# Kernel tuning notes

Hardware: AMD Instinct MI355X
Metric: run time of the kernel (lower is better)

The kernel has to match this reference:

```python
import jax, jax.numpy as jnp
import numpy as np
import math

HEAD_DIM = 128
THETA = 10000.0
MASK_VAL = -10000.0


def _rope(x, cos, sin):
    # x: (B, S, D); cos/sin: (S, D//2). Pairs (even, odd) rotated as complex.
    xr = x.reshape(*x.shape[:-1], -1, 2)
    xe, xo = xr[..., 0], xr[..., 1]
    oe = xe * cos - xo * sin
    oo = xe * sin + xo * cos
    return jnp.stack([oe, oo], axis=-1).reshape(x.shape)


def setup_inputs() -> dict:
    key = jax.random.key(0)
    B, S, D = 8, 4096, HEAD_DIM
    qkv = jax.random.normal(key, (B, S, 3 * D), dtype=jnp.float32)
    return {"qkv": qkv}


def reference(qkv):
    B, S, threeD = qkv.shape
    D = threeD // 3
    qkv = qkv.reshape(B, S, 3, D)
    q, k, v = qkv[:, :, 0], qkv[:, :, 1], qkv[:, :, 2]

    # precompute_freqs_cis: outer(t, 1/theta^(2i/d)) -> cos/sin (S, D//2)
    inv_freq = 1.0 / (THETA ** (jnp.arange(0, D, 2, dtype=jnp.float32) / D))
    freqs = jnp.arange(S, dtype=jnp.float32)[:, None] * inv_freq[None, :]
    cos, sin = jnp.cos(freqs), jnp.sin(freqs)
    q = _rope(q, cos, sin)
    k = _rope(k, cos, sin)

    scale = 1.0 / math.sqrt(D)
    scores = jnp.einsum('btd,bsd->bts', q, k) * scale  # (B, S, S)
    causal_mask = jnp.triu(jnp.full((S, S), MASK_VAL, dtype=scores.dtype), 1)
    attn = jax.nn.softmax(scores + causal_mask, axis=-1)
    out = jnp.einsum('bts,bsd->btd', attn, v)  # (B, S, D)
    return out
```

## Files before the change

kernel.cpp:

```cpp
#include <hip/hip_runtime.h>
#include <math.h>

typedef _Float16 half8 __attribute__((ext_vector_type(8)));
typedef float floatx4 __attribute__((ext_vector_type(4)));
typedef float floatx2 __attribute__((ext_vector_type(2)));

#define B_ 8
#define S_ 4096
#define SCALE_L2E 0.12751743008389106f
#define MASK_L2E  -14426.950408889634f
#define L2_10K_OVER_128 0.10381025296522975f

#define PLD 72
#define KW  136
#define VW  24
#define OSTLD 136
#define SLOTS_PER_B 576

__device__ __forceinline__ int chunk_prefix(int qt32) {
    int g = qt32 >> 4;
    return qt32 + 8 * g * (g - 1) + (qt32 - (g << 4)) * g;
}

__global__ __launch_bounds__(256) void prep_kernel(const float* __restrict__ qkv,
                                                   _Float16* __restrict__ Qh,
                                                   _Float16* __restrict__ Kp,
                                                   _Float16* __restrict__ Vp) {
    __shared__ __align__(16) _Float16 Kl[16][KW];
    __shared__ __align__(16) _Float16 Vt[128][VW];
    const int tid = threadIdx.x;
    const int b   = blockIdx.y;
    const int s0  = blockIdx.x * 16;

#pragma unroll
    for (int it = 0; it < 4; ++it) {
        int idx = tid + it * 256;
        int i = idx & 63, sr = idx >> 6, s = s0 + sr;
        const float* base = qkv + ((size_t)(b * S_ + s)) * 384 + 2 * i;
        floatx2 q2 = *(const floatx2*)base;
        floatx2 k2 = *(const floatx2*)(base + 128);
        float inv = exp2f(-(float)(2 * i) * L2_10K_OVER_128);
        float ang = (float)s * inv;
        float sn, cs;
        __sincosf(ang, &sn, &cs);
        size_t oq = ((size_t)(b * S_ + s)) * 128 + 2 * i;
        Qh[oq]     = (_Float16)((q2[0] * cs - q2[1] * sn) * SCALE_L2E);
        Qh[oq + 1] = (_Float16)((q2[0] * sn + q2[1] * cs) * SCALE_L2E);
        Kl[sr][2 * i]     = (_Float16)(k2[0] * cs - k2[1] * sn);
        Kl[sr][2 * i + 1] = (_Float16)(k2[0] * sn + k2[1] * cs);
    }
#pragma unroll
    for (int it = 0; it < 2; ++it) {
        int idx = tid + it * 256;
        int c = idx & 31, sr = idx >> 5;
        floatx4 v = *(const floatx4*)(qkv + ((size_t)(b * S_ + s0 + sr)) * 384 + 256 + c * 4);
#pragma unroll
        for (int j = 0; j < 4; ++j) Vt[c * 4 + j][sr] = (_Float16)v[j];
    }
    __syncthreads();

    {
        int c = tid >> 6, lane = tid & 63;
        int quad = lane >> 4, n = lane & 15;
        half8 val = *(const half8*)&Kl[n][c * 32 + quad * 8];
        int s16 = s0 >> 4;
        *(half8*)(Kp + (((size_t)(b * 256 + s16) * 4 + c) * 64 + lane) * 8) = val;
    }
    {
        int kt = s0 >> 6, c2 = (s0 >> 5) & 1, qp = (s0 >> 4) & 1;
        int nt = tid >> 5, lq = (tid >> 4) & 1, n = tid & 15;
        int quad = qp * 2 + lq;
        int lane = quad * 16 + n;
        half8 val = *(const half8*)&Vt[nt * 16 + n][lq * 8];
        *(half8*)(Vp + ((((size_t)(b * 64 + kt) * 2 + c2) * 8 + nt) * 64 + lane) * 8) = val;
    }
}

__global__ __launch_bounds__(64) void attn_part_kernel(const _Float16* __restrict__ Qh,
                                                       const _Float16* __restrict__ Kp,
                                                       const _Float16* __restrict__ Vp,
                                                       _Float16* __restrict__ Ppart,
                                                       float* __restrict__ Lpart) {
    __shared__ __align__(16) _Float16 SH[4 * 16 * PLD];

    const int lane  = threadIdx.x;
    const int quad  = lane >> 4;
    const int l16   = lane & 15;
    const int b     = blockIdx.x & 7;
    const int chunk = blockIdx.x >> 3;
    const int qt32  = 127 - blockIdx.y;
    const int qr0   = qt32 * 32;
    const int kt_max = (qr0 + 31) >> 6;
    const int c0    = chunk * 8;
    if (c0 > kt_max) return;
    const int kend  = min(kt_max, c0 + 7);
    const int slot  = b * SLOTS_PER_B + chunk_prefix(qt32) + chunk;

    half8 aq[2][4];
#pragma unroll
    for (int tile = 0; tile < 2; ++tile) {
        const _Float16* Qb = Qh + ((size_t)(b * S_) + qr0 + tile * 16 + l16) * 128;
#pragma unroll
        for (int c = 0; c < 4; ++c) aq[tile][c] = *(const half8*)(Qb + c * 32 + quad * 8);
    }

    floatx4 o[2][8];
#pragma unroll
    for (int tile = 0; tile < 2; ++tile)
#pragma unroll
        for (int i = 0; i < 8; ++i) o[tile][i] = (floatx4){0.f, 0.f, 0.f, 0.f};
    float rsum[2][4] = {{0.f, 0.f, 0.f, 0.f}, {0.f, 0.f, 0.f, 0.f}};

    const _Float16* Kb = Kp + (size_t)b * 524288;
    const _Float16* Vb = Vp + (size_t)b * 524288;

    for (int kt = c0; kt <= kend; ++kt) {
        floatx4 s4[2][4];
#pragma unroll
        for (int t = 0; t < 4; ++t) {
            const _Float16* kp = Kb + (((size_t)(kt * 16 + t * 4)) * 64 + lane) * 8;
            half8 bk[4];
#pragma unroll
            for (int c = 0; c < 4; ++c) bk[c] = *(const half8*)(kp + c * 512);
            floatx4 a0 = (floatx4){0.f, 0.f, 0.f, 0.f};
            floatx4 a1 = (floatx4){0.f, 0.f, 0.f, 0.f};
#pragma unroll
            for (int c = 0; c < 4; ++c) {
                a0 = __builtin_amdgcn_mfma_f32_16x16x32_f16(aq[0][c], bk[c], a0, 0, 0, 0);
                a1 = __builtin_amdgcn_mfma_f32_16x16x32_f16(aq[1][c], bk[c], a1, 0, 0, 0);
            }
            s4[0][t] = a0; s4[1][t] = a1;
        }

        if (kt == kt_max) {
#pragma unroll
            for (int tile = 0; tile < 2; ++tile)
#pragma unroll
                for (int t = 0; t < 4; ++t)
#pragma unroll
                    for (int r = 0; r < 4; ++r) {
                        int kcol = kt * 64 + t * 16 + l16;
                        int qr   = qr0 + tile * 16 + quad * 4 + r;
                        if (kcol > qr) s4[tile][t][r] += MASK_L2E;
                    }
        }

        const int buf = kt & 1;
#pragma unroll
        for (int tile = 0; tile < 2; ++tile)
#pragma unroll
            for (int t = 0; t < 4; ++t)
#pragma unroll
                for (int r = 0; r < 4; ++r) {
                    float p = __builtin_amdgcn_exp2f(s4[tile][t][r]);
                    rsum[tile][r] += p;
                    SH[(tile * 2 + buf) * (16 * PLD) + (quad * 4 + r) * PLD + t * 16 + l16] = (_Float16)p;
                }

#pragma unroll
        for (int c2 = 0; c2 < 2; ++c2) {
            half8 vf[8];
#pragma unroll
            for (int nt = 0; nt < 8; ++nt)
                vf[nt] = *(const half8*)(Vb + (((size_t)(kt * 2 + c2) * 8 + nt) * 64 + lane) * 8);
#pragma unroll
            for (int tile = 0; tile < 2; ++tile) {
                half8 ap = *(const half8*)&SH[(tile * 2 + buf) * (16 * PLD) + l16 * PLD + c2 * 32 + quad * 8];
#pragma unroll
                for (int nt = 0; nt < 8; ++nt)
                    o[tile][nt] = __builtin_amdgcn_mfma_f32_16x16x32_f16(ap, vf[nt], o[tile][nt], 0, 0, 0);
            }
        }
    }

#pragma unroll
    for (int off = 1; off <= 8; off <<= 1)
#pragma unroll
        for (int tile = 0; tile < 2; ++tile)
#pragma unroll
            for (int r = 0; r < 4; ++r)
                rsum[tile][r] += __shfl_xor(rsum[tile][r], off, 64);
    if (l16 == 0) {
#pragma unroll
        for (int tile = 0; tile < 2; ++tile)
#pragma unroll
            for (int r = 0; r < 4; ++r)
                Lpart[(size_t)slot * 32 + tile * 16 + quad * 4 + r] = rsum[tile][r];
    }

    _Float16* Ost = SH;
#pragma unroll
    for (int tile = 0; tile < 2; ++tile)
#pragma unroll
        for (int nt = 0; nt < 8; ++nt)
#pragma unroll
            for (int r = 0; r < 4; ++r)
                Ost[(tile * 16 + quad * 4 + r) * OSTLD + nt * 16 + l16] = (_Float16)o[tile][nt][r];
    _Float16* pp = Ppart + (size_t)slot * 4096;
#pragma unroll
    for (int i = 0; i < 8; ++i) {
        int idx = lane + i * 64;
        half8 v = *(const half8*)&Ost[(idx >> 4) * OSTLD + (idx & 15) * 8];
        *(half8*)(pp + (size_t)idx * 8) = v;
    }
}

__global__ __launch_bounds__(256) void reduce_kernel(const _Float16* __restrict__ Ppart,
                                                     const float* __restrict__ Lpart,
                                                     float* __restrict__ out) {
    const int bid  = blockIdx.x;
    const int b    = bid >> 7;
    const int qt32 = bid & 127;
    const int qr0  = qt32 * 32;
    const int nch  = (((qr0 + 31) >> 6) >> 3) + 1;
    const int slot0 = b * SLOTS_PER_B + chunk_prefix(qt32);
    const _Float16* pp = Ppart + (size_t)slot0 * 4096;
    const float* lp = Lpart + (size_t)slot0 * 32;
    const int tid = threadIdx.x;

#pragma unroll
    for (int j = 0; j < 2; ++j) {
        int idx = tid + j * 256;
        int row = idx >> 4;
        float acc[8] = {0.f, 0.f, 0.f, 0.f, 0.f, 0.f, 0.f, 0.f};
        float l = 0.f;
        for (int c = 0; c < nch; ++c) {
            half8 v = *(const half8*)(pp + (size_t)c * 4096 + (size_t)idx * 8);
#pragma unroll
            for (int k = 0; k < 8; ++k) acc[k] += (float)v[k];
            l += lp[c * 32 + row];
        }
        float inv = 1.0f / l;
        float* ob = out + ((size_t)(b * S_) + qr0) * 128 + (size_t)idx * 8;
        floatx4 o0 = (floatx4){acc[0] * inv, acc[1] * inv, acc[2] * inv, acc[3] * inv};
        floatx4 o1 = (floatx4){acc[4] * inv, acc[5] * inv, acc[6] * inv, acc[7] * inv};
        *(floatx4*)ob = o0;
        *(floatx4*)(ob + 4) = o1;
    }
}

__global__ __launch_bounds__(64) void attn_atomic_kernel(const _Float16* __restrict__ Qh,
                                                         const _Float16* __restrict__ Kp,
                                                         const _Float16* __restrict__ Vp,
                                                         float* __restrict__ out,
                                                         float* __restrict__ Lg) {
    __shared__ __align__(16) _Float16 Pl[2][16 * PLD];
    const int lane = threadIdx.x, quad = lane >> 4, l16 = lane & 15;
    const int b = blockIdx.x & 7, chunk = blockIdx.x >> 3;
    const int qt = 255 - blockIdx.y, qr0 = qt * 16;
    const int kt_max = qt >> 2, c0 = chunk * 8;
    if (c0 > kt_max) return;
    const int kend = min(kt_max, c0 + 7);
    const _Float16* Qb = Qh + ((size_t)(b * S_) + qr0 + l16) * 128;
    half8 aq[4];
#pragma unroll
    for (int c = 0; c < 4; ++c) aq[c] = *(const half8*)(Qb + c * 32 + quad * 8);
    floatx4 o[8];
#pragma unroll
    for (int i = 0; i < 8; ++i) o[i] = (floatx4){0.f, 0.f, 0.f, 0.f};
    float rsum[4] = {0.f, 0.f, 0.f, 0.f};
    const _Float16* Kb = Kp + (size_t)b * 524288;
    const _Float16* Vb = Vp + (size_t)b * 524288;
    for (int kt = c0; kt <= kend; ++kt) {
        half8 vf[2][8];
#pragma unroll
        for (int c2 = 0; c2 < 2; ++c2)
#pragma unroll
            for (int nt = 0; nt < 8; ++nt)
                vf[c2][nt] = *(const half8*)(Vb + (((size_t)(kt * 2 + c2) * 8 + nt) * 64 + lane) * 8);
        floatx4 s4[4];
#pragma unroll
        for (int t = 0; t < 4; ++t) {
            const _Float16* kp = Kb + ((size_t)((kt * 4 + t) * 4) * 64 + lane) * 8;
            floatx4 acc = (floatx4){0.f, 0.f, 0.f, 0.f};
#pragma unroll
            for (int c = 0; c < 4; ++c) {
                half8 bk = *(const half8*)(kp + c * 512);
                acc = __builtin_amdgcn_mfma_f32_16x16x32_f16(aq[c], bk, acc, 0, 0, 0);
            }
            s4[t] = acc;
        }
        if (kt == kt_max) {
#pragma unroll
            for (int t = 0; t < 4; ++t)
#pragma unroll
                for (int r = 0; r < 4; ++r) {
                    int kcol = kt * 64 + t * 16 + l16;
                    int qr = qr0 + quad * 4 + r;
                    if (kcol > qr) s4[t][r] += MASK_L2E;
                }
        }
        const int buf = kt & 1;
#pragma unroll
        for (int t = 0; t < 4; ++t)
#pragma unroll
            for (int r = 0; r < 4; ++r) {
                float p = __builtin_amdgcn_exp2f(s4[t][r]);
                rsum[r] += p;
                Pl[buf][(quad * 4 + r) * PLD + t * 16 + l16] = (_Float16)p;
            }
#pragma unroll
        for (int c2 = 0; c2 < 2; ++c2) {
            half8 ap = *(const half8*)&Pl[buf][l16 * PLD + c2 * 32 + quad * 8];
#pragma unroll
            for (int nt = 0; nt < 8; ++nt)
                o[nt] = __builtin_amdgcn_mfma_f32_16x16x32_f16(ap, vf[c2][nt], o[nt], 0, 0, 0);
        }
    }
#pragma unroll
    for (int off = 1; off <= 8; off <<= 1)
#pragma unroll
        for (int r = 0; r < 4; ++r)
            rsum[r] += __shfl_xor(rsum[r], off, 64);
    if (l16 == 0) {
#pragma unroll
        for (int r = 0; r < 4; ++r)
            atomicAdd(&Lg[(size_t)(b * S_) + qr0 + quad * 4 + r], rsum[r]);
    }
    float* ob = out + ((size_t)(b * S_) + qr0) * 128;
#pragma unroll
    for (int nt = 0; nt < 8; ++nt)
#pragma unroll
        for (int r = 0; r < 4; ++r)
            atomicAdd(&ob[(quad * 4 + r) * 128 + nt * 16 + l16], o[nt][r]);
}

__global__ __launch_bounds__(256) void norm_kernel(float* __restrict__ out,
                                                   const float* __restrict__ Lg) {
    int i = blockIdx.x * 256 + threadIdx.x;
    int row = i >> 5;
    floatx4 v = *(floatx4*)(out + (size_t)i * 4);
    float inv = 1.0f / Lg[row];
    v[0] *= inv; v[1] *= inv; v[2] *= inv; v[3] *= inv;
    *(floatx4*)(out + (size_t)i * 4) = v;
}

extern "C" void kernel_launch(void* const* d_in, const int* in_sizes, int n_in,
                              void* d_out, int out_size, void* d_ws, size_t ws_size,
                              hipStream_t stream) {
    const float* qkv = (const float*)d_in[0];
    float* out = (float*)d_out;
    const size_t MB = 1024 * 1024;
    _Float16* Qh = (_Float16*)d_ws;
    _Float16* Kp = (_Float16*)((char*)d_ws + 8 * MB);
    _Float16* Vp = (_Float16*)((char*)d_ws + 16 * MB);

    const size_t lpart_bytes = (size_t)B_ * SLOTS_PER_B * 32 * sizeof(float);
    const size_t ppart_bytes = (size_t)B_ * SLOTS_PER_B * 4096 * sizeof(_Float16);
    const size_t need = 25 * MB + ppart_bytes;

    prep_kernel<<<dim3(256, B_), dim3(256), 0, stream>>>(qkv, Qh, Kp, Vp);

    if (ws_size >= need) {
        float*    Lpart = (float*)((char*)d_ws + 24 * MB);
        _Float16* Ppart = (_Float16*)((char*)d_ws + 25 * MB);
        (void)lpart_bytes;
        attn_part_kernel<<<dim3(64, 128), dim3(64), 0, stream>>>(Qh, Kp, Vp, Ppart, Lpart);
        reduce_kernel<<<dim3(1024), dim3(256), 0, stream>>>(Ppart, Lpart, out);
    } else {
        float* Lg = (float*)((char*)d_ws + 24 * MB);
        hipMemsetAsync(out, 0, (size_t)B_ * S_ * 128 * sizeof(float), stream);
        hipMemsetAsync(Lg, 0, (size_t)B_ * S_ * sizeof(float), stream);
        attn_atomic_kernel<<<dim3(64, 256), dim3(64), 0, stream>>>(Qh, Kp, Vp, out, Lg);
        norm_kernel<<<dim3(4096), dim3(256), 0, stream>>>(out, Lg);
    }
}
```

Measured before the change: 167.9 us.

## Pack four attention waves per block and widen prep to 32 rows

The attention partial kernel now runs four independent 64-lane waves per 256-thread block. Each wave gets its own shared-memory slice and takes its batch/chunk from blockIdx.x*4+wid, so there are fewer blocks to launch and the work lands on compute units more densely. The double-buffered P staging is dropped to a single buffer per wave, and the output staging is done one tile at a time to fit that smaller slice. The prep kernel now handles 32 rows per 512-thread block, which lets V be written out as full 32-row fragments. Waves in a block exit early on their own, so some blocks may sit partly idle, and the single P buffer removes any overlap between writing P and reading it.

```diff
diff --git a/kernel.cpp b/kernel.cpp
--- a/kernel.cpp
+++ b/kernel.cpp
@@ -13,7 +13,7 @@
 
 #define PLD 72
 #define KW  136
-#define VW  24
+#define VW  40
 #define OSTLD 136
 #define SLOTS_PER_B 576
 
@@ -22,19 +22,19 @@
     return qt32 + 8 * g * (g - 1) + (qt32 - (g << 4)) * g;
 }
 
-__global__ __launch_bounds__(256) void prep_kernel(const float* __restrict__ qkv,
+__global__ __launch_bounds__(512) void prep_kernel(const float* __restrict__ qkv,
                                                    _Float16* __restrict__ Qh,
                                                    _Float16* __restrict__ Kp,
                                                    _Float16* __restrict__ Vp) {
-    __shared__ __align__(16) _Float16 Kl[16][KW];
+    __shared__ __align__(16) _Float16 Kl[32][KW];
     __shared__ __align__(16) _Float16 Vt[128][VW];
     const int tid = threadIdx.x;
     const int b   = blockIdx.y;
-    const int s0  = blockIdx.x * 16;
+    const int s0  = blockIdx.x * 32;
 
 #pragma unroll
     for (int it = 0; it < 4; ++it) {
-        int idx = tid + it * 256;
+        int idx = tid + it * 512;
         int i = idx & 63, sr = idx >> 6, s = s0 + sr;
         const float* base = qkv + ((size_t)(b * S_ + s)) * 384 + 2 * i;
         floatx2 q2 = *(const floatx2*)base;
@@ -51,7 +51,7 @@
     }
 #pragma unroll
     for (int it = 0; it < 2; ++it) {
-        int idx = tid + it * 256;
+        int idx = tid + it * 512;
         int c = idx & 31, sr = idx >> 5;
         floatx4 v = *(const floatx4*)(qkv + ((size_t)(b * S_ + s0 + sr)) * 384 + 256 + c * 4);
 #pragma unroll
@@ -60,34 +60,36 @@
     __syncthreads();
 
     {
-        int c = tid >> 6, lane = tid & 63;
+        int t = tid >> 8, c = (tid >> 6) & 3, lane = tid & 63;
         int quad = lane >> 4, n = lane & 15;
-        half8 val = *(const half8*)&Kl[n][c * 32 + quad * 8];
-        int s16 = s0 >> 4;
+        half8 val = *(const half8*)&Kl[t * 16 + n][c * 32 + quad * 8];
+        int s16 = (s0 >> 4) + t;
         *(half8*)(Kp + (((size_t)(b * 256 + s16) * 4 + c) * 64 + lane) * 8) = val;
     }
     {
-        int kt = s0 >> 6, c2 = (s0 >> 5) & 1, qp = (s0 >> 4) & 1;
-        int nt = tid >> 5, lq = (tid >> 4) & 1, n = tid & 15;
-        int quad = qp * 2 + lq;
-        int lane = quad * 16 + n;
-        half8 val = *(const half8*)&Vt[nt * 16 + n][lq * 8];
+        int kt = s0 >> 6, c2 = (s0 >> 5) & 1;
+        int nt = tid >> 6, lane = tid & 63;
+        int quad = lane >> 4, n = lane & 15;
+        half8 val = *(const half8*)&Vt[nt * 16 + n][quad * 8];
         *(half8*)(Vp + ((((size_t)(b * 64 + kt) * 2 + c2) * 8 + nt) * 64 + lane) * 8) = val;
     }
 }
 
-__global__ __launch_bounds__(64) void attn_part_kernel(const _Float16* __restrict__ Qh,
-                                                       const _Float16* __restrict__ Kp,
-                                                       const _Float16* __restrict__ Vp,
-                                                       _Float16* __restrict__ Ppart,
-                                                       float* __restrict__ Lpart) {
-    __shared__ __align__(16) _Float16 SH[4 * 16 * PLD];
-
-    const int lane  = threadIdx.x;
+__global__ __launch_bounds__(256) void attn_part_kernel(const _Float16* __restrict__ Qh,
+                                                        const _Float16* __restrict__ Kp,
+                                                        const _Float16* __restrict__ Vp,
+                                                        _Float16* __restrict__ Ppart,
+                                                        float* __restrict__ Lpart) {
+    __shared__ __align__(16) _Float16 SH[4][2 * 16 * PLD];
+
+    const int tid   = threadIdx.x;
+    const int wid   = tid >> 6;
+    const int lane  = tid & 63;
     const int quad  = lane >> 4;
     const int l16   = lane & 15;
-    const int b     = blockIdx.x & 7;
-    const int chunk = blockIdx.x >> 3;
+    const int ux    = blockIdx.x * 4 + wid;
+    const int b     = ux >> 3;
+    const int chunk = ux & 7;
     const int qt32  = 127 - blockIdx.y;
     const int qr0   = qt32 * 32;
     const int kt_max = (qr0 + 31) >> 6;
@@ -95,6 +97,7 @@
     if (c0 > kt_max) return;
     const int kend  = min(kt_max, c0 + 7);
     const int slot  = b * SLOTS_PER_B + chunk_prefix(qt32) + chunk;
+    _Float16* sh = SH[wid];
 
     half8 aq[2][4];
 #pragma unroll
@@ -145,7 +148,6 @@
                     }
         }
 
-        const int buf = kt & 1;
 #pragma unroll
         for (int tile = 0; tile < 2; ++tile)
 #pragma unroll
@@ -154,7 +156,7 @@
                 for (int r = 0; r < 4; ++r) {
                     float p = __builtin_amdgcn_exp2f(s4[tile][t][r]);
                     rsum[tile][r] += p;
-                    SH[(tile * 2 + buf) * (16 * PLD) + (quad * 4 + r) * PLD + t * 16 + l16] = (_Float16)p;
+                    sh[tile * (16 * PLD) + (quad * 4 + r) * PLD + t * 16 + l16] = (_Float16)p;
                 }
 
 #pragma unroll
@@ -165,7 +167,7 @@
                 vf[nt] = *(const half8*)(Vb + (((size_t)(kt * 2 + c2) * 8 + nt) * 64 + lane) * 8);
 #pragma unroll
             for (int tile = 0; tile < 2; ++tile) {
-                half8 ap = *(const half8*)&SH[(tile * 2 + buf) * (16 * PLD) + l16 * PLD + c2 * 32 + quad * 8];
+                half8 ap = *(const half8*)&sh[tile * (16 * PLD) + l16 * PLD + c2 * 32 + quad * 8];
 #pragma unroll
                 for (int nt = 0; nt < 8; ++nt)
                     o[tile][nt] = __builtin_amdgcn_mfma_f32_16x16x32_f16(ap, vf[nt], o[tile][nt], 0, 0, 0);
@@ -188,20 +190,21 @@
                 Lpart[(size_t)slot * 32 + tile * 16 + quad * 4 + r] = rsum[tile][r];
     }
 
-    _Float16* Ost = SH;
-#pragma unroll
-    for (int tile = 0; tile < 2; ++tile)
+    _Float16* Ost = sh;
+    _Float16* pp = Ppart + (size_t)slot * 4096;
+#pragma unroll
+    for (int tile = 0; tile < 2; ++tile) {
 #pragma unroll
         for (int nt = 0; nt < 8; ++nt)
 #pragma unroll
             for (int r = 0; r < 4; ++r)
-                Ost[(tile * 16 + quad * 4 + r) * OSTLD + nt * 16 + l16] = (_Float16)o[tile][nt][r];
-    _Float16* pp = Ppart + (size_t)slot * 4096;
-#pragma unroll
-    for (int i = 0; i < 8; ++i) {
-        int idx = lane + i * 64;
-        half8 v = *(const half8*)&Ost[(idx >> 4) * OSTLD + (idx & 15) * 8];
-        *(half8*)(pp + (size_t)idx * 8) = v;
+                Ost[(quad * 4 + r) * OSTLD + nt * 16 + l16] = (_Float16)o[tile][nt][r];
+#pragma unroll
+        for (int i = 0; i < 4; ++i) {
+            int idx = lane + i * 64;
+            half8 v = *(const half8*)&Ost[(idx >> 4) * OSTLD + (idx & 15) * 8];
+            *(half8*)(pp + (size_t)(tile * 2048 + idx * 8)) = v;
+        }
     }
 }
 
@@ -345,17 +348,15 @@
     _Float16* Kp = (_Float16*)((char*)d_ws + 8 * MB);
     _Float16* Vp = (_Float16*)((char*)d_ws + 16 * MB);
 
-    const size_t lpart_bytes = (size_t)B_ * SLOTS_PER_B * 32 * sizeof(float);
     const size_t ppart_bytes = (size_t)B_ * SLOTS_PER_B * 4096 * sizeof(_Float16);
     const size_t need = 25 * MB + ppart_bytes;
 
-    prep_kernel<<<dim3(256, B_), dim3(256), 0, stream>>>(qkv, Qh, Kp, Vp);
+    prep_kernel<<<dim3(128, B_), dim3(512), 0, stream>>>(qkv, Qh, Kp, Vp);
 
     if (ws_size >= need) {
         float*    Lpart = (float*)((char*)d_ws + 24 * MB);
         _Float16* Ppart = (_Float16*)((char*)d_ws + 25 * MB);
-        (void)lpart_bytes;
-        attn_part_kernel<<<dim3(64, 128), dim3(64), 0, stream>>>(Qh, Kp, Vp, Ppart, Lpart);
+        attn_part_kernel<<<dim3(16, 128), dim3(256), 0, stream>>>(Qh, Kp, Vp, Ppart, Lpart);
         reduce_kernel<<<dim3(1024), dim3(256), 0, stream>>>(Ppart, Lpart, out);
     } else {
         float* Lg = (float*)((char*)d_ws + 24 * MB);
```

New measurement: 194.1 us. 1.16x slower.

## Group four query tiles per block and prefetch V before QK compute

Applied to the files above, without the earlier changes.

Each block now runs four waves, each handling one 32-row query tile from a group of four consecutive tiles that share a key range, so K/V tiles are reused across waves through cache. V fragments for a key tile are loaded before the QK MFMAs to hide load latency. Waves whose diagonal lies earlier still iterate to the block's last key tile with masking, which adds some wasted MFMA and exp work. Output staging through LDS is done per tile to fit four per-wave buffers.

```diff
diff --git a/kernel.cpp b/kernel.cpp
--- a/kernel.cpp
+++ b/kernel.cpp
@@ -76,25 +76,31 @@
     }
 }
 
-__global__ __launch_bounds__(64) void attn_part_kernel(const _Float16* __restrict__ Qh,
-                                                       const _Float16* __restrict__ Kp,
-                                                       const _Float16* __restrict__ Vp,
-                                                       _Float16* __restrict__ Ppart,
-                                                       float* __restrict__ Lpart) {
-    __shared__ __align__(16) _Float16 SH[4 * 16 * PLD];
-
-    const int lane  = threadIdx.x;
+__global__ __launch_bounds__(256) void attn_part_kernel(const _Float16* __restrict__ Qh,
+                                                        const _Float16* __restrict__ Kp,
+                                                        const _Float16* __restrict__ Vp,
+                                                        _Float16* __restrict__ Ppart,
+                                                        float* __restrict__ Lpart) {
+    __shared__ __align__(16) _Float16 SH[4][4 * 16 * PLD];
+
+    const int tid   = threadIdx.x;
+    const int wid   = tid >> 6;
+    const int lane  = tid & 63;
     const int quad  = lane >> 4;
     const int l16   = lane & 15;
     const int b     = blockIdx.x & 7;
     const int chunk = blockIdx.x >> 3;
-    const int qt32  = 127 - blockIdx.y;
+    const int Q     = 31 - blockIdx.y;
+    const int nch   = (Q >> 2) + 1;
+    if (chunk >= nch) return;
+    const int qt32  = Q * 4 + wid;
     const int qr0   = qt32 * 32;
-    const int kt_max = (qr0 + 31) >> 6;
+    const int my_ktmax  = qt32 >> 1;
+    const int blk_ktmax = 2 * Q + 1;
     const int c0    = chunk * 8;
-    if (c0 > kt_max) return;
-    const int kend  = min(kt_max, c0 + 7);
+    const int kend  = min(blk_ktmax, c0 + 7);
     const int slot  = b * SLOTS_PER_B + chunk_prefix(qt32) + chunk;
+    _Float16* sh = SH[wid];
 
     half8 aq[2][4];
 #pragma unroll
@@ -115,6 +121,13 @@
     const _Float16* Vb = Vp + (size_t)b * 524288;
 
     for (int kt = c0; kt <= kend; ++kt) {
+        half8 vf[2][8];
+#pragma unroll
+        for (int c2 = 0; c2 < 2; ++c2)
+#pragma unroll
+            for (int nt = 0; nt < 8; ++nt)
+                vf[c2][nt] = *(const half8*)(Vb + (((size_t)(kt * 2 + c2) * 8 + nt) * 64 + lane) * 8);
+
         floatx4 s4[2][4];
 #pragma unroll
         for (int t = 0; t < 4; ++t) {
@@ -132,7 +145,7 @@
             s4[0][t] = a0; s4[1][t] = a1;
         }
 
-        if (kt == kt_max) {
+        if (kt >= my_ktmax) {
 #pragma unroll
             for (int tile = 0; tile < 2; ++tile)
 #pragma unroll
@@ -154,21 +167,17 @@
                 for (int r = 0; r < 4; ++r) {
                     float p = __builtin_amdgcn_exp2f(s4[tile][t][r]);
                     rsum[tile][r] += p;
-                    SH[(tile * 2 + buf) * (16 * PLD) + (quad * 4 + r) * PLD + t * 16 + l16] = (_Float16)p;
+                    sh[(tile * 2 + buf) * (16 * PLD) + (quad * 4 + r) * PLD + t * 16 + l16] = (_Float16)p;
                 }
 
 #pragma unroll
         for (int c2 = 0; c2 < 2; ++c2) {
-            half8 vf[8];
-#pragma unroll
-            for (int nt = 0; nt < 8; ++nt)
-                vf[nt] = *(const half8*)(Vb + (((size_t)(kt * 2 + c2) * 8 + nt) * 64 + lane) * 8);
 #pragma unroll
             for (int tile = 0; tile < 2; ++tile) {
-                half8 ap = *(const half8*)&SH[(tile * 2 + buf) * (16 * PLD) + l16 * PLD + c2 * 32 + quad * 8];
+                half8 ap = *(const half8*)&sh[(tile * 2 + buf) * (16 * PLD) + l16 * PLD + c2 * 32 + quad * 8];
 #pragma unroll
                 for (int nt = 0; nt < 8; ++nt)
-                    o[tile][nt] = __builtin_amdgcn_mfma_f32_16x16x32_f16(ap, vf[nt], o[tile][nt], 0, 0, 0);
+                    o[tile][nt] = __builtin_amdgcn_mfma_f32_16x16x32_f16(ap, vf[c2][nt], o[tile][nt], 0, 0, 0);
             }
         }
     }
@@ -188,20 +197,21 @@
                 Lpart[(size_t)slot * 32 + tile * 16 + quad * 4 + r] = rsum[tile][r];
     }
 
-    _Float16* Ost = SH;
-#pragma unroll
-    for (int tile = 0; tile < 2; ++tile)
+    _Float16* Ost = sh;
+    _Float16* pp = Ppart + (size_t)slot * 4096;
+#pragma unroll
+    for (int tile = 0; tile < 2; ++tile) {
 #pragma unroll
         for (int nt = 0; nt < 8; ++nt)
 #pragma unroll
             for (int r = 0; r < 4; ++r)
-                Ost[(tile * 16 + quad * 4 + r) * OSTLD + nt * 16 + l16] = (_Float16)o[tile][nt][r];
-    _Float16* pp = Ppart + (size_t)slot * 4096;
-#pragma unroll
-    for (int i = 0; i < 8; ++i) {
-        int idx = lane + i * 64;
-        half8 v = *(const half8*)&Ost[(idx >> 4) * OSTLD + (idx & 15) * 8];
-        *(half8*)(pp + (size_t)idx * 8) = v;
+                Ost[(quad * 4 + r) * OSTLD + nt * 16 + l16] = (_Float16)o[tile][nt][r];
+#pragma unroll
+        for (int i = 0; i < 4; ++i) {
+            int idx = lane + i * 64;
+            half8 v = *(const half8*)&Ost[(idx >> 4) * OSTLD + (idx & 15) * 8];
+            *(half8*)(pp + (size_t)(tile * 2048 + idx * 8)) = v;
+        }
     }
 }
 
@@ -212,7 +222,7 @@
     const int b    = bid >> 7;
     const int qt32 = bid & 127;
     const int qr0  = qt32 * 32;
-    const int nch  = (((qr0 + 31) >> 6) >> 3) + 1;
+    const int nch  = (qt32 >> 4) + 1;
     const int slot0 = b * SLOTS_PER_B + chunk_prefix(qt32);
     const _Float16* pp = Ppart + (size_t)slot0 * 4096;
     const float* lp = Lpart + (size_t)slot0 * 32;
@@ -345,7 +355,6 @@
     _Float16* Kp = (_Float16*)((char*)d_ws + 8 * MB);
     _Float16* Vp = (_Float16*)((char*)d_ws + 16 * MB);
 
-    const size_t lpart_bytes = (size_t)B_ * SLOTS_PER_B * 32 * sizeof(float);
     const size_t ppart_bytes = (size_t)B_ * SLOTS_PER_B * 4096 * sizeof(_Float16);
     const size_t need = 25 * MB + ppart_bytes;
 
@@ -354,8 +363,7 @@
     if (ws_size >= need) {
         float*    Lpart = (float*)((char*)d_ws + 24 * MB);
         _Float16* Ppart = (_Float16*)((char*)d_ws + 25 * MB);
-        (void)lpart_bytes;
-        attn_part_kernel<<<dim3(64, 128), dim3(64), 0, stream>>>(Qh, Kp, Vp, Ppart, Lpart);
+        attn_part_kernel<<<dim3(64, 32), dim3(256), 0, stream>>>(Qh, Kp, Vp, Ppart, Lpart);
         reduce_kernel<<<dim3(1024), dim3(256), 0, stream>>>(Ppart, Lpart, out);
     } else {
         float* Lg = (float*)((char*)d_ws + 24 * MB);
```

After: 185.0 us. 10.2% more time.
